# Kernel tuning notes

Hardware: AMD Instinct MI355X
Metric: run time of the kernel (lower is better)

## Reference

```python
import jax, jax.numpy as jnp
import numpy as np

EMBED_DIM = 1024
NUM_HEADS = 16
HEAD_DIM = EMBED_DIM // NUM_HEADS


def setup_inputs() -> dict:
    key = jax.random.key(0)
    ks = jax.random.split(key, 7)
    B, L, E = 2, 2048, EMBED_DIM
    scale = 1.0 / np.sqrt(E)
    x = jax.random.normal(ks[0], (B, L, E), dtype=jnp.float32)
    Wq = jax.random.normal(ks[1], (E, E), dtype=jnp.float32) * scale
    Wk = jax.random.normal(ks[2], (E, E), dtype=jnp.float32) * scale
    Wv = jax.random.normal(ks[3], (E, E), dtype=jnp.float32) * scale
    bq = jax.random.normal(ks[4], (E,), dtype=jnp.float32) * 0.01
    bk = jax.random.normal(ks[5], (E,), dtype=jnp.float32) * 0.01
    bv = jax.random.normal(ks[6], (E,), dtype=jnp.float32) * 0.01
    return {"x": x, "Wq": Wq, "bq": bq, "Wk": Wk, "bk": bk, "Wv": Wv, "bv": bv}


def reference(x, Wq, bq, Wk, bk, Wv, bv):
    B, L, E = x.shape
    H, D = NUM_HEADS, HEAD_DIM

    def proj(W, b):
        # [B,L,E] -> [B,H,L,D]
        return (x @ W + b).reshape(B, L, H, D).transpose(0, 2, 1, 3)

    q = proj(Wq, bq)
    k = proj(Wk, bk)
    v = proj(Wv, bv)
    # scores: [B,H,L,M]; NOTE: no 1/sqrt(d) scaling in the original
    scores = jnp.einsum('bhld,bhmd->bhlm', q, k)
    # softmax over the QUERY axis (dim=2), matching scores.softmax(dim=2)
    weights = jax.nn.softmax(scores, axis=2)
    out = jnp.einsum('bhlm,bhmd->bhld', weights, v)
    return out.transpose(0, 2, 1, 3).reshape(B, L, E)
```

## Files before the change

kernel.cpp:

```cpp
#include <hip/hip_runtime.h>


typedef _Float16 f16x8 __attribute__((ext_vector_type(8)));
typedef _Float16 f16x4 __attribute__((ext_vector_type(4)));
typedef __fp16 fp16x2 __attribute__((ext_vector_type(2)));
typedef float f32x4 __attribute__((ext_vector_type(4)));

#define MFMA(a, b, c) __builtin_amdgcn_mfma_f32_16x16x32_f16((a), (b), (c), 0, 0, 0)
#define EXP2(x) __builtin_amdgcn_exp2f(x)
#define LOG2E 1.44269504088896340736f

__global__ __launch_bounds__(256) void k_convert_x(const float* __restrict__ x,
                                                   _Float16* __restrict__ xb) {
    int i = (blockIdx.x * 256 + threadIdx.x) * 4;
    float4 f = *(const float4*)(x + i);
    f16x4 o = {(_Float16)f.x, (_Float16)f.y, (_Float16)f.z, (_Float16)f.w};
    *(f16x4*)(xb + i) = o;
}

__global__ __launch_bounds__(256) void k_convert_wt(const float* __restrict__ Wq,
                                                    const float* __restrict__ Wk,
                                                    const float* __restrict__ Wv,
                                                    _Float16* __restrict__ wbt) {
    const int jz = blockIdx.z;
    const float* W = (jz == 0) ? Wq : (jz == 1) ? Wk : Wv;
    __shared__ float tile[64][65];
    const int k0 = blockIdx.y * 64, n0 = blockIdx.x * 64;
    for (int e = threadIdx.x; e < 4096; e += 256) {
        int r = e >> 6, c = e & 63;
        tile[r][c] = W[(k0 + r) * 1024 + n0 + c];
    }
    __syncthreads();
    for (int e = threadIdx.x; e < 4096; e += 256) {
        int r = e >> 6, c = e & 63;
        wbt[((size_t)jz * 1024 + n0 + r) * 1024 + k0 + c] = (_Float16)tile[c][r];
    }
}

__global__ __launch_bounds__(256) void k_proj_gemm(const _Float16* __restrict__ xb,
                                                   const _Float16* __restrict__ wbt,
                                                   const float* __restrict__ bq,
                                                   const float* __restrict__ bk,
                                                   const float* __restrict__ bv,
                                                   _Float16* __restrict__ Qb,
                                                   _Float16* __restrict__ Kb,
                                                   _Float16* __restrict__ Vt) {
    const int n0 = blockIdx.x * 128;
    const int m0 = blockIdx.y * 128;
    __shared__ _Float16 As[128][40];
    __shared__ _Float16 Bs[128][40];
    const int tid = threadIdx.x;
    const int lane = tid & 63, wv = tid >> 6;
    const int l15 = lane & 15, quad = lane >> 4;
    const int wr = wv >> 1, wc = wv & 1;

    f32x4 acc[4][4] = {};
    for (int k0 = 0; k0 < 1024; k0 += 32) {
        __syncthreads();
        for (int j = 0; j < 2; ++j) {
            int chunk = tid + 256 * j;
            int row = chunk >> 2, c = chunk & 3;
            *(uint4*)&As[row][c * 8] = *(const uint4*)&xb[(size_t)(m0 + row) * 1024 + k0 + c * 8];
            *(uint4*)&Bs[row][c * 8] = *(const uint4*)&wbt[(size_t)(n0 + row) * 1024 + k0 + c * 8];
        }
        __syncthreads();
        f16x8 af[4], bf[4];
        for (int i = 0; i < 4; ++i) {
            af[i] = *(const f16x8*)&As[wr * 64 + i * 16 + l15][quad * 8];
            bf[i] = *(const f16x8*)&Bs[wc * 64 + i * 16 + l15][quad * 8];
        }
        for (int i = 0; i < 4; ++i)
            for (int j = 0; j < 4; ++j)
                acc[i][j] = MFMA(af[i], bf[j], acc[i][j]);
    }

    const int proj = n0 >> 10;
    const float* bias = (proj == 0) ? bq : (proj == 1) ? bk : bv;
    const float scale = (proj == 0) ? LOG2E : 1.0f;
    for (int j = 0; j < 4; ++j) {
        int n = n0 + wc * 64 + j * 16 + l15;
        int nn = n & 1023;
        float bsv = bias[nn];
        int h = nn >> 6, d = nn & 63;
        for (int i = 0; i < 4; ++i) {
            for (int r = 0; r < 4; ++r) {
                int t = m0 + wr * 64 + i * 16 + quad * 4 + r;
                int b = t >> 11, l = t & 2047;
                _Float16 val = (_Float16)((acc[i][j][r] + bsv) * scale);
                int bh = b * 16 + h;
                if (proj == 0)
                    Qb[((size_t)bh * 2048 + l) * 64 + d] = val;
                else if (proj == 1)
                    Kb[((size_t)bh * 2048 + l) * 64 + d] = val;
                else
                    Vt[((size_t)bh * 64 + d) * 2048 + l] = val;
            }
        }
    }
}

__global__ __launch_bounds__(256, 1) void k_stats(const _Float16* __restrict__ Qb,
                                                  const _Float16* __restrict__ Kb,
                                                  float* __restrict__ d2) {
    const int id = blockIdx.x;
    const int wk = (id & 7) * 32 + (id >> 3);
    const int bh = wk >> 3;
    const int mt = wk & 7;
    const int lane = threadIdx.x & 63, wv = threadIdx.x >> 6;
    const int l15 = lane & 15, quad = lane >> 4;
    const int m0 = mt * 256 + wv * 64;
    const size_t base = (size_t)bh * 2048 * 64;
    const _Float16* Kp = Kb + base;
    const _Float16* Qp = Qb + base;

    f16x8 bf[4][2];
    #pragma unroll
    for (int s = 0; s < 4; ++s) {
        bf[s][0] = *(const f16x8*)&Kp[(size_t)(m0 + s * 16 + l15) * 64 + quad * 8];
        bf[s][1] = *(const f16x8*)&Kp[(size_t)(m0 + s * 16 + l15) * 64 + 32 + quad * 8];
    }
    float rs[4] = {0.f, 0.f, 0.f, 0.f};
    f16x8 qc[2][2], qn[2][2];
    #pragma unroll
    for (int lt = 0; lt < 2; ++lt) {
        qc[lt][0] = *(const f16x8*)&Qp[(size_t)(lt * 16 + l15) * 64 + quad * 8];
        qc[lt][1] = *(const f16x8*)&Qp[(size_t)(lt * 16 + l15) * 64 + 32 + quad * 8];
    }
    for (int l0 = 0; l0 < 2048; l0 += 32) {
        int l1 = (l0 + 32) & 2047;
        #pragma unroll
        for (int lt = 0; lt < 2; ++lt) {
            qn[lt][0] = *(const f16x8*)&Qp[(size_t)(l1 + lt * 16 + l15) * 64 + quad * 8];
            qn[lt][1] = *(const f16x8*)&Qp[(size_t)(l1 + lt * 16 + l15) * 64 + 32 + quad * 8];
        }
        #pragma unroll
        for (int s = 0; s < 4; ++s)
            #pragma unroll
            for (int lt = 0; lt < 2; ++lt) {
                f32x4 a = {};
                a = MFMA(qc[lt][0], bf[s][0], a);
                a = MFMA(qc[lt][1], bf[s][1], a);
                rs[s] += EXP2(a[0]) + EXP2(a[1]) + EXP2(a[2]) + EXP2(a[3]);
            }
        #pragma unroll
        for (int lt = 0; lt < 2; ++lt) {
            qc[lt][0] = qn[lt][0];
            qc[lt][1] = qn[lt][1];
        }
    }
    #pragma unroll
    for (int s = 0; s < 4; ++s) {
        rs[s] += __shfl_xor(rs[s], 16, 64);
        rs[s] += __shfl_xor(rs[s], 32, 64);
    }
    float myz = (quad == 0) ? rs[0] : (quad == 1) ? rs[1] : (quad == 2) ? rs[2] : rs[3];
    d2[bh * 2048 + m0 + quad * 16 + l15] = __builtin_amdgcn_logf(myz);
}

__global__ __launch_bounds__(256, 1) void k_attn(const _Float16* __restrict__ Qb,
                                                 const _Float16* __restrict__ Kb,
                                                 const _Float16* __restrict__ Vt,
                                                 const float* __restrict__ d2,
                                                 float* __restrict__ out) {
    __shared__ _Float16 Ps[4][64][40];
    const int id = blockIdx.x;
    const int wk = (id & 7) * 32 + (id >> 3);
    const int bh = wk >> 3;
    const int ltile = wk & 7;
    const int b = bh >> 4, h = bh & 15;
    const int lane = threadIdx.x & 63, wv = threadIdx.x >> 6;
    const int l15 = lane & 15, quad = lane >> 4;
    const int l0 = ltile * 256 + wv * 64;
    const size_t base = (size_t)bh * 2048 * 64;
    const _Float16* Qp = Qb + base;
    const _Float16* Kp = Kb + base;
    const _Float16* Vp = Vt + base;
    const float* d2p = d2 + bh * 2048;

    f16x8 qf[4][2];
    #pragma unroll
    for (int lt = 0; lt < 4; ++lt) {
        qf[lt][0] = *(const f16x8*)&Qp[(size_t)(l0 + lt * 16 + l15) * 64 + quad * 8];
        qf[lt][1] = *(const f16x8*)&Qp[(size_t)(l0 + lt * 16 + l15) * 64 + 32 + quad * 8];
    }
    f32x4 oacc[4][4] = {};

    f16x8 kf[2][2], nkf[2][2], vf[4], nvf[4];
    f32x4 dv[2], ndv[2];
    #pragma unroll
    for (int s = 0; s < 2; ++s) {
        kf[s][0] = *(const f16x8*)&Kp[(size_t)(s * 16 + l15) * 64 + quad * 8];
        kf[s][1] = *(const f16x8*)&Kp[(size_t)(s * 16 + l15) * 64 + 32 + quad * 8];
        dv[s] = *(const f32x4*)&d2p[s * 16 + quad * 4];
    }
    #pragma unroll
    for (int dt = 0; dt < 4; ++dt)
        vf[dt] = *(const f16x8*)&Vp[(size_t)(dt * 16 + l15) * 2048 + quad * 8];

    for (int m0 = 0; m0 < 2048; m0 += 32) {
        const int m1 = (m0 + 32) & 2047;
        #pragma unroll
        for (int s = 0; s < 2; ++s) {
            nkf[s][0] = *(const f16x8*)&Kp[(size_t)(m1 + s * 16 + l15) * 64 + quad * 8];
            nkf[s][1] = *(const f16x8*)&Kp[(size_t)(m1 + s * 16 + l15) * 64 + 32 + quad * 8];
            ndv[s] = *(const f32x4*)&d2p[m1 + s * 16 + quad * 4];
        }
        #pragma unroll
        for (int dt = 0; dt < 4; ++dt)
            nvf[dt] = *(const f16x8*)&Vp[(size_t)(dt * 16 + l15) * 2048 + m1 + quad * 8];
        #pragma unroll
        for (int s = 0; s < 2; ++s)
            #pragma unroll
            for (int lt = 0; lt < 4; ++lt) {
                f32x4 a = {};
                a = MFMA(kf[s][0], qf[lt][0], a);
                a = MFMA(kf[s][1], qf[lt][1], a);
                union { fp16x2 h[2]; f16x4 v; } u;
                u.h[0] = __builtin_amdgcn_cvt_pkrtz(EXP2(a[0] - dv[s][0]),
                                                    EXP2(a[1] - dv[s][1]));
                u.h[1] = __builtin_amdgcn_cvt_pkrtz(EXP2(a[2] - dv[s][2]),
                                                    EXP2(a[3] - dv[s][3]));
                *(f16x4*)&Ps[wv][lt * 16 + l15][s * 16 + quad * 4] = u.v;
            }
        #pragma unroll
        for (int lt = 0; lt < 4; ++lt) {
            f16x8 pf = *(const f16x8*)&Ps[wv][lt * 16 + l15][quad * 8];
            #pragma unroll
            for (int dt = 0; dt < 4; ++dt)
                oacc[dt][lt] = MFMA(vf[dt], pf, oacc[dt][lt]);
        }
        #pragma unroll
        for (int s = 0; s < 2; ++s) {
            kf[s][0] = nkf[s][0];
            kf[s][1] = nkf[s][1];
            dv[s] = ndv[s];
        }
        #pragma unroll
        for (int dt = 0; dt < 4; ++dt) vf[dt] = nvf[dt];
    }
    #pragma unroll
    for (int lt = 0; lt < 4; ++lt)
        #pragma unroll
        for (int dt = 0; dt < 4; ++dt) {
            int l = l0 + lt * 16 + l15;
            float4 o4 = {oacc[dt][lt][0], oacc[dt][lt][1], oacc[dt][lt][2], oacc[dt][lt][3]};
            *(float4*)&out[((size_t)(b * 2048 + l)) * 1024 + h * 64 + dt * 16 + quad * 4] = o4;
        }
}

extern "C" void kernel_launch(void* const* d_in, const int* in_sizes, int n_in,
                              void* d_out, int out_size, void* d_ws, size_t ws_size,
                              hipStream_t stream) {
    const float* x  = (const float*)d_in[0];
    const float* Wq = (const float*)d_in[1];
    const float* bq = (const float*)d_in[2];
    const float* Wk = (const float*)d_in[3];
    const float* bk = (const float*)d_in[4];
    const float* Wv = (const float*)d_in[5];
    const float* bv = (const float*)d_in[6];
    float* out = (float*)d_out;

    char* w = (char*)d_ws;
    _Float16* xb  = (_Float16*)(w);
    _Float16* wbt = (_Float16*)(w + (size_t)(8 << 20));
    _Float16* Qb  = (_Float16*)(w + (size_t)(14 << 20));
    _Float16* Kb  = (_Float16*)(w + (size_t)(22 << 20));
    _Float16* Vt  = (_Float16*)(w + (size_t)(30 << 20));
    float* d2     = (float*)(w + (size_t)(38 << 20));

    k_convert_x<<<4096, 256, 0, stream>>>(x, xb);
    k_convert_wt<<<dim3(16, 16, 3), 256, 0, stream>>>(Wq, Wk, Wv, wbt);
    k_proj_gemm<<<dim3(24, 32), 256, 0, stream>>>(xb, wbt, bq, bk, bv, Qb, Kb, Vt);
    k_stats<<<256, 256, 0, stream>>>(Qb, Kb, d2);
    k_attn<<<256, 256, 0, stream>>>(Qb, Kb, Vt, d2, out);
}
```

Baseline: 254.3 us.

## Split key/query reduction across waves to launch 4x more blocks for stats and attention

The stats and attention kernels now give each block a 64-row tile, with the four waves each covering a quarter of the reduction axis (512 rows) instead of separate row tiles. This raises the grid from 256 to 1024 blocks and sets launch bounds to 4 blocks per CU, so more waves are resident and latency is better hidden on a device with 256 CUs. The cost is cross-wave reductions through shared memory plus barriers. The attention epilogue is serialized over four dt steps with two syncs each and adds shared-memory pressure from the obuf staging buffer.

```diff
diff --git a/kernel.cpp b/kernel.cpp
--- a/kernel.cpp
+++ b/kernel.cpp
@@ -99,16 +99,18 @@
     }
 }
 
-__global__ __launch_bounds__(256, 1) void k_stats(const _Float16* __restrict__ Qb,
+__global__ __launch_bounds__(256, 4) void k_stats(const _Float16* __restrict__ Qb,
                                                   const _Float16* __restrict__ Kb,
                                                   float* __restrict__ d2) {
+    __shared__ float sred[4][4][64];
     const int id = blockIdx.x;
-    const int wk = (id & 7) * 32 + (id >> 3);
-    const int bh = wk >> 3;
-    const int mt = wk & 7;
+    const int wk = (id & 7) * 128 + (id >> 3);
+    const int bh = wk >> 5;
+    const int mt = wk & 31;
     const int lane = threadIdx.x & 63, wv = threadIdx.x >> 6;
     const int l15 = lane & 15, quad = lane >> 4;
-    const int m0 = mt * 256 + wv * 64;
+    const int m0 = mt * 64;
+    const int lbase = wv * 512;
     const size_t base = (size_t)bh * 2048 * 64;
     const _Float16* Kp = Kb + base;
     const _Float16* Qp = Qb + base;
@@ -123,11 +125,11 @@
     f16x8 qc[2][2], qn[2][2];
     #pragma unroll
     for (int lt = 0; lt < 2; ++lt) {
-        qc[lt][0] = *(const f16x8*)&Qp[(size_t)(lt * 16 + l15) * 64 + quad * 8];
-        qc[lt][1] = *(const f16x8*)&Qp[(size_t)(lt * 16 + l15) * 64 + 32 + quad * 8];
-    }
-    for (int l0 = 0; l0 < 2048; l0 += 32) {
-        int l1 = (l0 + 32) & 2047;
+        qc[lt][0] = *(const f16x8*)&Qp[(size_t)(lbase + lt * 16 + l15) * 64 + quad * 8];
+        qc[lt][1] = *(const f16x8*)&Qp[(size_t)(lbase + lt * 16 + l15) * 64 + 32 + quad * 8];
+    }
+    for (int lr = 0; lr < 512; lr += 32) {
+        int l1 = lbase + ((lr + 32) & 511);
         #pragma unroll
         for (int lt = 0; lt < 2; ++lt) {
             qn[lt][0] = *(const f16x8*)&Qp[(size_t)(l1 + lt * 16 + l15) * 64 + quad * 8];
@@ -149,28 +151,37 @@
         }
     }
     #pragma unroll
-    for (int s = 0; s < 4; ++s) {
-        rs[s] += __shfl_xor(rs[s], 16, 64);
-        rs[s] += __shfl_xor(rs[s], 32, 64);
-    }
-    float myz = (quad == 0) ? rs[0] : (quad == 1) ? rs[1] : (quad == 2) ? rs[2] : rs[3];
-    d2[bh * 2048 + m0 + quad * 16 + l15] = __builtin_amdgcn_logf(myz);
-}
-
-__global__ __launch_bounds__(256, 1) void k_attn(const _Float16* __restrict__ Qb,
+    for (int s = 0; s < 4; ++s) sred[wv][s][lane] = rs[s];
+    __syncthreads();
+    if (wv == 0) {
+        #pragma unroll
+        for (int s = 0; s < 4; ++s) {
+            float t = sred[0][s][lane] + sred[1][s][lane] + sred[2][s][lane] + sred[3][s][lane];
+            t += __shfl_xor(t, 16, 64);
+            t += __shfl_xor(t, 32, 64);
+            rs[s] = t;
+        }
+        float myz = (quad == 0) ? rs[0] : (quad == 1) ? rs[1] : (quad == 2) ? rs[2] : rs[3];
+        d2[bh * 2048 + m0 + quad * 16 + l15] = __builtin_amdgcn_logf(myz);
+    }
+}
+
+__global__ __launch_bounds__(256, 4) void k_attn(const _Float16* __restrict__ Qb,
                                                  const _Float16* __restrict__ Kb,
                                                  const _Float16* __restrict__ Vt,
                                                  const float* __restrict__ d2,
                                                  float* __restrict__ out) {
     __shared__ _Float16 Ps[4][64][40];
+    __shared__ f32x4 obuf[3][4][64];
     const int id = blockIdx.x;
-    const int wk = (id & 7) * 32 + (id >> 3);
-    const int bh = wk >> 3;
-    const int ltile = wk & 7;
+    const int wk = (id & 7) * 128 + (id >> 3);
+    const int bh = wk >> 5;
+    const int ltile = wk & 31;
     const int b = bh >> 4, h = bh & 15;
     const int lane = threadIdx.x & 63, wv = threadIdx.x >> 6;
     const int l15 = lane & 15, quad = lane >> 4;
-    const int l0 = ltile * 256 + wv * 64;
+    const int l0 = ltile * 64;
+    const int mbase = wv * 512;
     const size_t base = (size_t)bh * 2048 * 64;
     const _Float16* Qp = Qb + base;
     const _Float16* Kp = Kb + base;
@@ -189,16 +200,17 @@
     f32x4 dv[2], ndv[2];
     #pragma unroll
     for (int s = 0; s < 2; ++s) {
-        kf[s][0] = *(const f16x8*)&Kp[(size_t)(s * 16 + l15) * 64 + quad * 8];
-        kf[s][1] = *(const f16x8*)&Kp[(size_t)(s * 16 + l15) * 64 + 32 + quad * 8];
-        dv[s] = *(const f32x4*)&d2p[s * 16 + quad * 4];
+        kf[s][0] = *(const f16x8*)&Kp[(size_t)(mbase + s * 16 + l15) * 64 + quad * 8];
+        kf[s][1] = *(const f16x8*)&Kp[(size_t)(mbase + s * 16 + l15) * 64 + 32 + quad * 8];
+        dv[s] = *(const f32x4*)&d2p[mbase + s * 16 + quad * 4];
     }
     #pragma unroll
     for (int dt = 0; dt < 4; ++dt)
-        vf[dt] = *(const f16x8*)&Vp[(size_t)(dt * 16 + l15) * 2048 + quad * 8];
-
-    for (int m0 = 0; m0 < 2048; m0 += 32) {
-        const int m1 = (m0 + 32) & 2047;
+        vf[dt] = *(const f16x8*)&Vp[(size_t)(dt * 16 + l15) * 2048 + mbase + quad * 8];
+
+    for (int mr = 0; mr < 512; mr += 32) {
+        const int m0 = mbase + mr;
+        const int m1 = mbase + ((mr + 32) & 511);
         #pragma unroll
         for (int s = 0; s < 2; ++s) {
             nkf[s][0] = *(const f16x8*)&Kp[(size_t)(m1 + s * 16 + l15) * 64 + quad * 8];
@@ -239,13 +251,23 @@
         for (int dt = 0; dt < 4; ++dt) vf[dt] = nvf[dt];
     }
     #pragma unroll
-    for (int lt = 0; lt < 4; ++lt)
-        #pragma unroll
-        for (int dt = 0; dt < 4; ++dt) {
-            int l = l0 + lt * 16 + l15;
-            float4 o4 = {oacc[dt][lt][0], oacc[dt][lt][1], oacc[dt][lt][2], oacc[dt][lt][3]};
-            *(float4*)&out[((size_t)(b * 2048 + l)) * 1024 + h * 64 + dt * 16 + quad * 4] = o4;
-        }
+    for (int dt = 0; dt < 4; ++dt) {
+        if (wv > 0) {
+            #pragma unroll
+            for (int lt = 0; lt < 4; ++lt) obuf[wv - 1][lt][lane] = oacc[dt][lt];
+        }
+        __syncthreads();
+        if (wv == 0) {
+            #pragma unroll
+            for (int lt = 0; lt < 4; ++lt) {
+                f32x4 o = oacc[dt][lt] + obuf[0][lt][lane] + obuf[1][lt][lane] + obuf[2][lt][lane];
+                int l = l0 + lt * 16 + l15;
+                float4 o4 = {o[0], o[1], o[2], o[3]};
+                *(float4*)&out[((size_t)(b * 2048 + l)) * 1024 + h * 64 + dt * 16 + quad * 4] = o4;
+            }
+        }
+        __syncthreads();
+    }
 }
 
 extern "C" void kernel_launch(void* const* d_in, const int* in_sizes, int n_in,
@@ -271,6 +293,6 @@
     k_convert_x<<<4096, 256, 0, stream>>>(x, xb);
     k_convert_wt<<<dim3(16, 16, 3), 256, 0, stream>>>(Wq, Wk, Wv, wbt);
     k_proj_gemm<<<dim3(24, 32), 256, 0, stream>>>(xb, wbt, bq, bk, bv, Qb, Kb, Vt);
-    k_stats<<<256, 256, 0, stream>>>(Qb, Kb, d2);
-    k_attn<<<256, 256, 0, stream>>>(Qb, Kb, Vt, d2, out);
-}
+    k_stats<<<1024, 256, 0, stream>>>(Qb, Kb, d2);
+    k_attn<<<1024, 256, 0, stream>>>(Qb, Kb, Vt, d2, out);
+}
```

Result: slower. 474.2 us (+86.5%).
